# Optimization experiments

Hardware: AMD Instinct MI355X
Metric: run time of the kernel (lower is better)

## Reference

```python
import jax, jax.numpy as jnp
import numpy as np

MUL_S, MUL_V = 256, 128              # 256x0e + 128x1o hidden irreps
DIM_H = MUL_S + 3 * MUL_V            # 640
N_NODES = 100000
INV_SQRT3 = 3.0 ** -0.5
# e3nn 'element' path normalization: sqrt(ir_out.dim / sum_paths(mul1*mul2));
# for the 1o output the extra sqrt(3) cancels the 1/sqrt(3) of the wigner-3j,
# so every path ends up with the same constant.
C0 = (1.0 / (MUL_S + MUL_V)) ** 0.5


def _unif(key, shape, fan):
    # matches linear_layer_init: uniform(-a, a), a = sqrt(6/(mul1*mul2 + mul_out)), mul2 = 1
    a = (6.0 / fan) ** 0.5
    return jax.random.uniform(key, shape, minval=-a, maxval=a, dtype=jnp.float32)


def setup_inputs() -> dict:
    key = jax.random.key(0)
    ks = jax.random.split(key, 8)
    data_in = jax.random.normal(ks[0], (N_NODES, DIM_H + 4), dtype=jnp.float32)
    return {
        "data_in": data_in,
        "W_ss": _unif(ks[1], (MUL_S, MUL_S), MUL_S + MUL_S),      # 0e x 0e -> 0e (scalars)
        "W_vv": _unif(ks[2], (MUL_V, MUL_S), MUL_V + MUL_S),      # 1o x 1o -> 0e (scalars)
        "W_ss_g": _unif(ks[3], (MUL_S, MUL_V), MUL_S + MUL_V),    # 0e x 0e -> 0e (gates)
        "W_vv_g": _unif(ks[4], (MUL_V, MUL_V), MUL_V + MUL_V),    # 1o x 1o -> 0e (gates)
        "W_sv": _unif(ks[5], (MUL_S, MUL_V), MUL_S + MUL_V),      # 0e x 1o -> 1o
        "W_vs": _unif(ks[6], (MUL_V, MUL_V), MUL_V + MUL_V),      # 1o x 0e -> 1o
        "b": jnp.zeros((MUL_S,), dtype=jnp.float32),
    }


def reference(data_in, W_ss, W_vv, W_ss_g, W_vv_g, W_sv, W_vs, b):
    # split hidden / pos parts (forward does data_in[:, :-irreps_pos.dim] etc.)
    xs = data_in[:, :MUL_S]                           # [N, 256] 0e
    xv = data_in[:, MUL_S:DIM_H].reshape(-1, MUL_V, 3)  # [N, 128, 3] 1o
    ps = data_in[:, DIM_H:DIM_H + 1]                  # [N, 1] pos scalar
    pv = data_in[:, DIM_H + 1:]                       # [N, 3] pos vector

    # CG invariants feeding the 0e outputs
    s0 = xs * ps                                       # 0e x 0e path
    dot = jnp.einsum('nuk,nk->nu', xv, pv) * INV_SQRT3  # 1o x 1o -> 0e path, [N, 128]

    scal = C0 * (s0 @ W_ss + dot @ W_vv) + b           # [N, 256] scalars (+bias on N_trivial)
    gate = C0 * (s0 @ W_ss_g + dot @ W_vv_g)           # [N, 128] gates

    # 1o outputs: 0e x 1o and 1o x 0e paths
    v1 = (xs @ W_sv)[:, :, None] * pv[:, None, :]            # [N, 128, 3]
    v2 = jnp.einsum('nuk,uw->nwk', xv, W_vs) * ps[:, :, None]  # [N, 128, 3]
    vec = C0 * (v1 + v2)

    # Gate: Swish(beta=1) on scalars, sigmoid(gates) multiplying gated 1o irreps
    scal_out = scal * jax.nn.sigmoid(scal)
    vec_out = vec * jax.nn.sigmoid(gate)[:, :, None]
    return jnp.concatenate([scal_out, vec_out.reshape(-1, 3 * MUL_V)], axis=1)  # [N, 640]
```

## Files before the change

kernel.cpp:

```cpp
#include <hip/hip_runtime.h>
#include <hip/hip_bf16.h>

#define MUL_Sc 256
#define DIM_Hc 640
#define IN_COLS 644
#define KF 768
#define NT 32

#define C0F 0.05103103630798287f
#define INV_SQRT3F 0.57735026918962576f

typedef __attribute__((ext_vector_type(8))) short short8;
typedef __attribute__((ext_vector_type(4))) float f32x4;

#define MFMA(a, b, c) __builtin_amdgcn_mfma_f32_16x16x32_bf16((a), (b), (c), 0, 0, 0)

__device__ __forceinline__ unsigned short f2bf(float x) {
    union { float f; unsigned u; } v; v.f = x;
    unsigned r = v.u + 0x7fffu + ((v.u >> 16) & 1u);
    return (unsigned short)(r >> 16);
}

__device__ __forceinline__ void gload_lds16(const unsigned short* g, unsigned short* l) {
    __builtin_amdgcn_global_load_lds((const __attribute__((address_space(1))) void*)g,
                                     (__attribute__((address_space(3))) void*)l, 16, 0, 0);
}

__global__ void prep_weights(const float* __restrict__ Wss, const float* __restrict__ Wvv,
                             const float* __restrict__ Wssg, const float* __restrict__ Wvvg,
                             const float* __restrict__ Wsv, const float* __restrict__ Wvs,
                             unsigned short* __restrict__ wt) {
    int i = blockIdx.x * 256 + threadIdx.x;
    const int N_SG = 384 * 384;
    const int N_SV = 128 * 256;
    const int N_VS = 128 * 128;
    if (i < N_SG) {
        int col = i / 384, k = i % 384;
        float v;
        if (col < 256) v = (k < 256) ? Wss[k * 256 + col] : Wvv[(k - 256) * 256 + col];
        else { int c = col - 256; v = (k < 256) ? Wssg[k * 128 + c] : Wvvg[(k - 256) * 128 + c]; }
        wt[i] = f2bf(v);
    } else if (i < N_SG + N_SV) {
        int j = i - N_SG; int col = j >> 8, k = j & 255;
        wt[i] = f2bf(Wsv[k * 128 + col]);
    } else if (i < N_SG + N_SV + N_VS) {
        int j = i - N_SG - N_SV; int col = j >> 7, k = j & 127;
        wt[i] = f2bf(Wvs[k * 128 + col]);
    }
}

__global__ __launch_bounds__(512, 2)
void fused_main(const float* __restrict__ din, const unsigned short* __restrict__ wt,
                const float* __restrict__ bias, float* __restrict__ out, int N) {
    __shared__ unsigned short feat[NT * KF];
    __shared__ unsigned short ldsB[2][384 * 64];
    __shared__ float psv[NT * 4];

    const int tid  = threadIdx.x;
    const int wave = tid >> 6;
    const int lane = tid & 63;
    const int n0   = blockIdx.x * NT;

    const unsigned short* WTsg = wt;
    const unsigned short* WTsv = wt + 384 * 384;
    const unsigned short* WTvs = wt + 384 * 384 + 128 * 256;

    auto stage = [&](int buf, const unsigned short* W, int rs, int nr, int step) {
        unsigned short* lb = &ldsB[buf][0] + wave * 512;
        #pragma unroll
        for (int m = 0; m < nr; ++m) {
            int slot = m * 512 + tid;
            int col  = slot >> 3;
            int k8   = (slot & 7) ^ (col & 7);
            gload_lds16(W + col * rs + step * 64 + k8 * 8, lb + m * 4096);
        }
    };

    stage(0, WTsg, 384, 6, 0);

    {
        const int g = tid >> 4;
        const int j = tid & 15;
        int n = n0 + g; if (n >= N) n = N - 1;
        const float* row = din + (size_t)n * IN_COLS;
        float ps  = row[DIM_Hc];
        float pv0 = row[DIM_Hc + 1], pv1 = row[DIM_Hc + 2], pv2 = row[DIM_Hc + 3];
        if (j == 0) { psv[g*4+0] = ps; psv[g*4+1] = pv0; psv[g*4+2] = pv1; psv[g*4+3] = pv2; }
        char* fb = (char*)feat;
        const int swz  = (g & 7) << 4;
        const int rowb = g * (KF * 2);

        {
            int c = 16 * j;
            float4 x0 = *(const float4*)(row + c);
            float4 x1 = *(const float4*)(row + c + 4);
            float4 x2 = *(const float4*)(row + c + 8);
            float4 x3 = *(const float4*)(row + c + 12);
            short8 p0, p1;
            p0[0]=(short)f2bf(x0.x); p0[1]=(short)f2bf(x0.y); p0[2]=(short)f2bf(x0.z); p0[3]=(short)f2bf(x0.w);
            p0[4]=(short)f2bf(x1.x); p0[5]=(short)f2bf(x1.y); p0[6]=(short)f2bf(x1.z); p0[7]=(short)f2bf(x1.w);
            p1[0]=(short)f2bf(x2.x); p1[1]=(short)f2bf(x2.y); p1[2]=(short)f2bf(x2.z); p1[3]=(short)f2bf(x2.w);
            p1[4]=(short)f2bf(x3.x); p1[5]=(short)f2bf(x3.y); p1[6]=(short)f2bf(x3.z); p1[7]=(short)f2bf(x3.w);
            *(short8*)(fb + ((rowb + c * 2) ^ swz))       = p0;
            *(short8*)(fb + ((rowb + (c + 8) * 2) ^ swz)) = p1;
        }
        {
            int u0 = 8 * j;
            const float* p = row + MUL_Sc + 3 * u0;
            float e[24];
            #pragma unroll
            for (int q = 0; q < 6; ++q) {
                float4 v = *(const float4*)(p + 4 * q);
                e[4*q+0] = v.x; e[4*q+1] = v.y; e[4*q+2] = v.z; e[4*q+3] = v.w;
            }
            short8 dp, k0, k1, k2;
            #pragma unroll
            for (int m = 0; m < 8; ++m) {
                float a = e[3*m], b = e[3*m+1], c = e[3*m+2];
                dp[m] = (short)f2bf((a * pv0 + b * pv1 + c * pv2) * INV_SQRT3F);
                k0[m] = (short)f2bf(a);
                k1[m] = (short)f2bf(b);
                k2[m] = (short)f2bf(c);
            }
            *(short8*)(fb + ((rowb + (256 + u0) * 2) ^ swz)) = dp;
            *(short8*)(fb + ((rowb + (384 + u0) * 2) ^ swz)) = k0;
            *(short8*)(fb + ((rowb + (512 + u0) * 2) ^ swz)) = k1;
            *(short8*)(fb + ((rowb + (640 + u0) * 2) ^ swz)) = k2;
        }
    }
    __syncthreads();

    const int l15   = lane & 15;
    const int lkb   = (lane >> 4) << 3;
    const int chnk  = lane >> 4;
    const int rbase = (lane >> 4) << 2;
    const char* fbr = (const char*)feat;
    const int swzr  = (l15 & 7) << 4;

    float pss[2][4];
    #pragma unroll
    for (int s = 0; s < 2; ++s)
    #pragma unroll
    for (int i = 0; i < 4; ++i) pss[s][i] = psv[(s * 16 + rbase + i) * 4];

    f32x4 accS[3][2];
    #pragma unroll
    for (int t = 0; t < 3; ++t) { accS[t][0] = (f32x4){0,0,0,0}; accS[t][1] = (f32x4){0,0,0,0}; }
    f32x4 accA[2];
    accA[0] = (f32x4){0,0,0,0}; accA[1] = (f32x4){0,0,0,0};
    f32x4 accV[3][2];
    #pragma unroll
    for (int k = 0; k < 3; ++k) { accV[k][0] = (f32x4){0,0,0,0}; accV[k][1] = (f32x4){0,0,0,0}; }

    auto sgstep = [&](int buf, int step) {
        const char* B = (const char*)&ldsB[buf][0];
        #pragma unroll
        for (int ks = 0; ks < 2; ++ks) {
            int kf = step * 64 + ks * 32 + lkb;
            short8 a0 = *(const short8*)(fbr + ((l15 * 1536 + kf * 2) ^ swzr));
            short8 a1 = *(const short8*)(fbr + (((16 + l15) * 1536 + kf * 2) ^ swzr));
            int ch = ks * 4 + chnk;
            #pragma unroll
            for (int t = 0; t < 3; ++t) {
                int col = (wave + t * 8) * 16 + l15;
                short8 b = *(const short8*)(B + col * 128 + ((ch ^ (col & 7)) << 4));
                accS[t][0] = MFMA(a0, b, accS[t][0]);
                accS[t][1] = MFMA(a1, b, accS[t][1]);
            }
        }
    };
    auto svstep = [&](int buf, int step) {
        const char* B = (const char*)&ldsB[buf][0];
        #pragma unroll
        for (int ks = 0; ks < 2; ++ks) {
            int kf = step * 64 + ks * 32 + lkb;
            short8 a0 = *(const short8*)(fbr + ((l15 * 1536 + kf * 2) ^ swzr));
            short8 a1 = *(const short8*)(fbr + (((16 + l15) * 1536 + kf * 2) ^ swzr));
            int ch = ks * 4 + chnk;
            int col = wave * 16 + l15;
            short8 b = *(const short8*)(B + col * 128 + ((ch ^ (col & 7)) << 4));
            accA[0] = MFMA(a0, b, accA[0]);
            accA[1] = MFMA(a1, b, accA[1]);
        }
    };
    auto vsstep = [&](int buf, int step) {
        const char* B = (const char*)&ldsB[buf][0];
        #pragma unroll
        for (int ks = 0; ks < 2; ++ks) {
            int ch = ks * 4 + chnk;
            int col = wave * 16 + l15;
            short8 b = *(const short8*)(B + col * 128 + ((ch ^ (col & 7)) << 4));
            #pragma unroll
            for (int p = 0; p < 3; ++p) {
                int kf = 384 + p * 128 + step * 64 + ks * 32 + lkb;
                short8 a0 = *(const short8*)(fbr + ((l15 * 1536 + kf * 2) ^ swzr));
                short8 a1 = *(const short8*)(fbr + (((16 + l15) * 1536 + kf * 2) ^ swzr));
                accV[p][0] = MFMA(a0, b, accV[p][0]);
                accV[p][1] = MFMA(a1, b, accV[p][1]);
            }
        }
    };

    stage(1, WTsg, 384, 6, 1);  sgstep(0, 0);  __syncthreads();
    stage(0, WTsg, 384, 6, 2);  sgstep(1, 1);  __syncthreads();
    stage(1, WTsg, 384, 6, 3);  sgstep(0, 2);  __syncthreads();
    stage(0, WTsg, 384, 6, 4);  sgstep(1, 3);
    #pragma unroll
    for (int t = 0; t < 3; ++t)
    #pragma unroll
    for (int s = 0; s < 2; ++s)
    #pragma unroll
    for (int i = 0; i < 4; ++i) accS[t][s][i] *= pss[s][i];
    __syncthreads();
    stage(1, WTsg, 384, 6, 5);  sgstep(0, 4);  __syncthreads();
    stage(0, WTsv, 256, 2, 0);  sgstep(1, 5);

    #pragma unroll
    for (int t = 0; t < 2; ++t) {
        int col = (wave + t * 8) * 16 + l15;
        float bc = bias[col];
        #pragma unroll
        for (int s = 0; s < 2; ++s)
        #pragma unroll
        for (int i = 0; i < 4; ++i) {
            int n = n0 + s * 16 + rbase + i;
            if (n < N) {
                float sc = C0F * accS[t][s][i] + bc;
                out[(size_t)n * DIM_Hc + col] = sc / (1.f + __expf(-sc));
            }
        }
    }
    float sgr[2][4];
    #pragma unroll
    for (int s = 0; s < 2; ++s)
    #pragma unroll
    for (int i = 0; i < 4; ++i) sgr[s][i] = 1.f / (1.f + __expf(-C0F * accS[2][s][i]));
    __syncthreads();

    stage(1, WTsv, 256, 2, 1);  svstep(0, 0);  __syncthreads();
    stage(0, WTsv, 256, 2, 2);  svstep(1, 1);  __syncthreads();
    stage(1, WTsv, 256, 2, 3);  svstep(0, 2);  __syncthreads();
    stage(0, WTvs, 128, 2, 0);  svstep(1, 3);  __syncthreads();
    stage(1, WTvs, 128, 2, 1);  vsstep(0, 0);  __syncthreads();
                                vsstep(1, 1);

    {
        int u = wave * 16 + l15;
        #pragma unroll
        for (int s = 0; s < 2; ++s)
        #pragma unroll
        for (int i = 0; i < 4; ++i) {
            int nl = s * 16 + rbase + i;
            int n = n0 + nl;
            if (n >= N) continue;
            float sg  = sgr[s][i];
            float ps  = pss[s][i];
            float pv0 = psv[nl * 4 + 1], pv1 = psv[nl * 4 + 2], pv2 = psv[nl * 4 + 3];
            float av = accA[s][i];
            size_t ob = (size_t)n * DIM_Hc + MUL_Sc + 3 * u;
            out[ob + 0] = C0F * (av * pv0 + accV[0][s][i] * ps) * sg;
            out[ob + 1] = C0F * (av * pv1 + accV[1][s][i] * ps) * sg;
            out[ob + 2] = C0F * (av * pv2 + accV[2][s][i] * ps) * sg;
        }
    }
}

extern "C" void kernel_launch(void* const* d_in, const int* in_sizes, int n_in,
                              void* d_out, int out_size, void* d_ws, size_t ws_size,
                              hipStream_t stream) {
    const float* din  = (const float*)d_in[0];
    const float* Wss  = (const float*)d_in[1];
    const float* Wvv  = (const float*)d_in[2];
    const float* Wssg = (const float*)d_in[3];
    const float* Wvvg = (const float*)d_in[4];
    const float* Wsv  = (const float*)d_in[5];
    const float* Wvs  = (const float*)d_in[6];
    const float* bias = (const float*)d_in[7];
    float* out = (float*)d_out;
    unsigned short* wt = (unsigned short*)d_ws;

    const size_t WT_BYTES = (size_t)(384 * 384 + 128 * 256 + 128 * 128) * 2;
    if (ws_size < WT_BYTES) return;

    int N = in_sizes[0] / IN_COLS;

    int prep_total = 384 * 384 + 128 * 256 + 128 * 128;
    prep_weights<<<(prep_total + 255) / 256, 256, 0, stream>>>(Wss, Wvv, Wssg, Wvvg, Wsv, Wvs, wt);

    int nblocks = (N + NT - 1) / NT;
    fused_main<<<nblocks, 512, 0, stream>>>(din, wt, bias, out, N);
}
```

Before: 269.3 us.

## Use persistent producer/consumer blocks with double-buffered feature tiles and direct global weight reads

Launches a fixed grid of 256 persistent blocks that loop over 32-node tiles. Half the threads act as producers, converting and staging the next tile's features into a second LDS buffer, while the other four waves run the MFMA work on the current tile. Weights are no longer staged through LDS; consumers read B fragments straight from global memory (L2/L1 cached), and each consumer wave now handles twice the columns. This aims to overlap input loading with compute and remove the per-step weight-staging barriers. In exchange, only half the threads issue MFMAs, and there is more global-load latency on the weight operand.

After: 333.8 us. +24.0%, slower.

```diff
diff --git a/kernel.cpp b/kernel.cpp
--- a/kernel.cpp
+++ b/kernel.cpp
@@ -6,6 +6,7 @@
 #define IN_COLS 644
 #define KF 768
 #define NT 32
+#define GRIDB 256
 
 #define C0F 0.05103103630798287f
 #define INV_SQRT3F 0.57735026918962576f
@@ -19,11 +20,6 @@
     union { float f; unsigned u; } v; v.f = x;
     unsigned r = v.u + 0x7fffu + ((v.u >> 16) & 1u);
     return (unsigned short)(r >> 16);
-}
-
-__device__ __forceinline__ void gload_lds16(const unsigned short* g, unsigned short* l) {
-    __builtin_amdgcn_global_load_lds((const __attribute__((address_space(1))) void*)g,
-                                     (__attribute__((address_space(3))) void*)l, 16, 0, 0);
 }
 
 __global__ void prep_weights(const float* __restrict__ Wss, const float* __restrict__ Wvv,
@@ -51,217 +47,229 @@
 
 __global__ __launch_bounds__(512, 2)
 void fused_main(const float* __restrict__ din, const unsigned short* __restrict__ wt,
-                const float* __restrict__ bias, float* __restrict__ out, int N) {
-    __shared__ unsigned short feat[NT * KF];
-    __shared__ unsigned short ldsB[2][384 * 64];
-    __shared__ float psv[NT * 4];
+                const float* __restrict__ bias, float* __restrict__ out,
+                int N, int ntiles) {
+    __shared__ unsigned short feat[2][NT * KF];
+    __shared__ float psv[2][NT * 4];
 
     const int tid  = threadIdx.x;
-    const int wave = tid >> 6;
-    const int lane = tid & 63;
-    const int n0   = blockIdx.x * NT;
+    const bool prod = tid >= 256;
+    const int ptid = tid & 255;
 
     const unsigned short* WTsg = wt;
     const unsigned short* WTsv = wt + 384 * 384;
     const unsigned short* WTvs = wt + 384 * 384 + 128 * 256;
 
-    auto stage = [&](int buf, const unsigned short* W, int rs, int nr, int step) {
-        unsigned short* lb = &ldsB[buf][0] + wave * 512;
+    const int cw    = tid >> 6;
+    const int lane  = tid & 63;
+    const int l15   = lane & 15;
+    const int lkb   = (lane >> 4) << 3;
+    const int rbase = (lane >> 4) << 2;
+    const int swzr  = (l15 & 7) << 4;
+
+    float bcs[4];
+    if (!prod) {
         #pragma unroll
-        for (int m = 0; m < nr; ++m) {
-            int slot = m * 512 + tid;
-            int col  = slot >> 3;
-            int k8   = (slot & 7) ^ (col & 7);
-            gload_lds16(W + col * rs + step * 64 + k8 * 8, lb + m * 4096);
+        for (int t = 0; t < 4; ++t) bcs[t] = bias[(t * 4 + cw) * 16 + l15];
+    }
+
+    auto stage_tile = [&](int tile, int wb) {
+        char* fb = (char*)&feat[wb][0];
+        #pragma unroll
+        for (int h = 0; h < 2; ++h) {
+            const int g = h * 16 + (ptid >> 4);
+            const int j = ptid & 15;
+            int n = tile * NT + g; if (n >= N) n = N - 1;
+            const float* row = din + (size_t)n * IN_COLS;
+            float ps  = row[DIM_Hc];
+            float pv0 = row[DIM_Hc + 1], pv1 = row[DIM_Hc + 2], pv2 = row[DIM_Hc + 3];
+            if (j == 0) {
+                psv[wb][g*4+0] = ps; psv[wb][g*4+1] = pv0;
+                psv[wb][g*4+2] = pv1; psv[wb][g*4+3] = pv2;
+            }
+            const int swz  = (g & 7) << 4;
+            const int rowb = g * (KF * 2);
+
+            {
+                int c = 16 * j;
+                float4 x0 = *(const float4*)(row + c);
+                float4 x1 = *(const float4*)(row + c + 4);
+                float4 x2 = *(const float4*)(row + c + 8);
+                float4 x3 = *(const float4*)(row + c + 12);
+                short8 p0, p1;
+                p0[0]=(short)f2bf(x0.x); p0[1]=(short)f2bf(x0.y); p0[2]=(short)f2bf(x0.z); p0[3]=(short)f2bf(x0.w);
+                p0[4]=(short)f2bf(x1.x); p0[5]=(short)f2bf(x1.y); p0[6]=(short)f2bf(x1.z); p0[7]=(short)f2bf(x1.w);
+                p1[0]=(short)f2bf(x2.x); p1[1]=(short)f2bf(x2.y); p1[2]=(short)f2bf(x2.z); p1[3]=(short)f2bf(x2.w);
+                p1[4]=(short)f2bf(x3.x); p1[5]=(short)f2bf(x3.y); p1[6]=(short)f2bf(x3.z); p1[7]=(short)f2bf(x3.w);
+                *(short8*)(fb + ((rowb + c * 2) ^ swz))       = p0;
+                *(short8*)(fb + ((rowb + (c + 8) * 2) ^ swz)) = p1;
+            }
+            {
+                int u0 = 8 * j;
+                const float* p = row + MUL_Sc + 3 * u0;
+                float e[24];
+                #pragma unroll
+                for (int q = 0; q < 6; ++q) {
+                    float4 v = *(const float4*)(p + 4 * q);
+                    e[4*q+0] = v.x; e[4*q+1] = v.y; e[4*q+2] = v.z; e[4*q+3] = v.w;
+                }
+                short8 dp, k0, k1, k2;
+                #pragma unroll
+                for (int m = 0; m < 8; ++m) {
+                    float a = e[3*m], b = e[3*m+1], c = e[3*m+2];
+                    dp[m] = (short)f2bf((a * pv0 + b * pv1 + c * pv2) * INV_SQRT3F);
+                    k0[m] = (short)f2bf(a);
+                    k1[m] = (short)f2bf(b);
+                    k2[m] = (short)f2bf(c);
+                }
+                *(short8*)(fb + ((rowb + (256 + u0) * 2) ^ swz)) = dp;
+                *(short8*)(fb + ((rowb + (384 + u0) * 2) ^ swz)) = k0;
+                *(short8*)(fb + ((rowb + (512 + u0) * 2) ^ swz)) = k1;
+                *(short8*)(fb + ((rowb + (640 + u0) * 2) ^ swz)) = k2;
+            }
         }
     };
 
-    stage(0, WTsg, 384, 6, 0);
-
-    {
-        const int g = tid >> 4;
-        const int j = tid & 15;
-        int n = n0 + g; if (n >= N) n = N - 1;
-        const float* row = din + (size_t)n * IN_COLS;
-        float ps  = row[DIM_Hc];
-        float pv0 = row[DIM_Hc + 1], pv1 = row[DIM_Hc + 2], pv2 = row[DIM_Hc + 3];
-        if (j == 0) { psv[g*4+0] = ps; psv[g*4+1] = pv0; psv[g*4+2] = pv1; psv[g*4+3] = pv2; }
-        char* fb = (char*)feat;
-        const int swz  = (g & 7) << 4;
-        const int rowb = g * (KF * 2);
-
-        {
-            int c = 16 * j;
-            float4 x0 = *(const float4*)(row + c);
-            float4 x1 = *(const float4*)(row + c + 4);
-            float4 x2 = *(const float4*)(row + c + 8);
-            float4 x3 = *(const float4*)(row + c + 12);
-            short8 p0, p1;
-            p0[0]=(short)f2bf(x0.x); p0[1]=(short)f2bf(x0.y); p0[2]=(short)f2bf(x0.z); p0[3]=(short)f2bf(x0.w);
-            p0[4]=(short)f2bf(x1.x); p0[5]=(short)f2bf(x1.y); p0[6]=(short)f2bf(x1.z); p0[7]=(short)f2bf(x1.w);
-            p1[0]=(short)f2bf(x2.x); p1[1]=(short)f2bf(x2.y); p1[2]=(short)f2bf(x2.z); p1[3]=(short)f2bf(x2.w);
-            p1[4]=(short)f2bf(x3.x); p1[5]=(short)f2bf(x3.y); p1[6]=(short)f2bf(x3.z); p1[7]=(short)f2bf(x3.w);
-            *(short8*)(fb + ((rowb + c * 2) ^ swz))       = p0;
-            *(short8*)(fb + ((rowb + (c + 8) * 2) ^ swz)) = p1;
-        }
-        {
-            int u0 = 8 * j;
-            const float* p = row + MUL_Sc + 3 * u0;
-            float e[24];
-            #pragma unroll
-            for (int q = 0; q < 6; ++q) {
-                float4 v = *(const float4*)(p + 4 * q);
-                e[4*q+0] = v.x; e[4*q+1] = v.y; e[4*q+2] = v.z; e[4*q+3] = v.w;
-            }
-            short8 dp, k0, k1, k2;
-            #pragma unroll
-            for (int m = 0; m < 8; ++m) {
-                float a = e[3*m], b = e[3*m+1], c = e[3*m+2];
-                dp[m] = (short)f2bf((a * pv0 + b * pv1 + c * pv2) * INV_SQRT3F);
-                k0[m] = (short)f2bf(a);
-                k1[m] = (short)f2bf(b);
-                k2[m] = (short)f2bf(c);
-            }
-            *(short8*)(fb + ((rowb + (256 + u0) * 2) ^ swz)) = dp;
-            *(short8*)(fb + ((rowb + (384 + u0) * 2) ^ swz)) = k0;
-            *(short8*)(fb + ((rowb + (512 + u0) * 2) ^ swz)) = k1;
-            *(short8*)(fb + ((rowb + (640 + u0) * 2) ^ swz)) = k2;
-        }
-    }
+    if (prod) stage_tile(blockIdx.x, 0);
     __syncthreads();
 
-    const int l15   = lane & 15;
-    const int lkb   = (lane >> 4) << 3;
-    const int chnk  = lane >> 4;
-    const int rbase = (lane >> 4) << 2;
-    const char* fbr = (const char*)feat;
-    const int swzr  = (l15 & 7) << 4;
-
-    float pss[2][4];
-    #pragma unroll
-    for (int s = 0; s < 2; ++s)
-    #pragma unroll
-    for (int i = 0; i < 4; ++i) pss[s][i] = psv[(s * 16 + rbase + i) * 4];
-
-    f32x4 accS[3][2];
-    #pragma unroll
-    for (int t = 0; t < 3; ++t) { accS[t][0] = (f32x4){0,0,0,0}; accS[t][1] = (f32x4){0,0,0,0}; }
-    f32x4 accA[2];
-    accA[0] = (f32x4){0,0,0,0}; accA[1] = (f32x4){0,0,0,0};
-    f32x4 accV[3][2];
-    #pragma unroll
-    for (int k = 0; k < 3; ++k) { accV[k][0] = (f32x4){0,0,0,0}; accV[k][1] = (f32x4){0,0,0,0}; }
-
-    auto sgstep = [&](int buf, int step) {
-        const char* B = (const char*)&ldsB[buf][0];
-        #pragma unroll
-        for (int ks = 0; ks < 2; ++ks) {
-            int kf = step * 64 + ks * 32 + lkb;
-            short8 a0 = *(const short8*)(fbr + ((l15 * 1536 + kf * 2) ^ swzr));
-            short8 a1 = *(const short8*)(fbr + (((16 + l15) * 1536 + kf * 2) ^ swzr));
-            int ch = ks * 4 + chnk;
-            #pragma unroll
-            for (int t = 0; t < 3; ++t) {
-                int col = (wave + t * 8) * 16 + l15;
-                short8 b = *(const short8*)(B + col * 128 + ((ch ^ (col & 7)) << 4));
-                accS[t][0] = MFMA(a0, b, accS[t][0]);
-                accS[t][1] = MFMA(a1, b, accS[t][1]);
-            }
-        }
-    };
-    auto svstep = [&](int buf, int step) {
-        const char* B = (const char*)&ldsB[buf][0];
-        #pragma unroll
-        for (int ks = 0; ks < 2; ++ks) {
-            int kf = step * 64 + ks * 32 + lkb;
-            short8 a0 = *(const short8*)(fbr + ((l15 * 1536 + kf * 2) ^ swzr));
-            short8 a1 = *(const short8*)(fbr + (((16 + l15) * 1536 + kf * 2) ^ swzr));
-            int ch = ks * 4 + chnk;
-            int col = wave * 16 + l15;
-            short8 b = *(const short8*)(B + col * 128 + ((ch ^ (col & 7)) << 4));
-            accA[0] = MFMA(a0, b, accA[0]);
-            accA[1] = MFMA(a1, b, accA[1]);
-        }
-    };
-    auto vsstep = [&](int buf, int step) {
-        const char* B = (const char*)&ldsB[buf][0];
-        #pragma unroll
-        for (int ks = 0; ks < 2; ++ks) {
-            int ch = ks * 4 + chnk;
-            int col = wave * 16 + l15;
-            short8 b = *(const short8*)(B + col * 128 + ((ch ^ (col & 7)) << 4));
-            #pragma unroll
-            for (int p = 0; p < 3; ++p) {
-                int kf = 384 + p * 128 + step * 64 + ks * 32 + lkb;
+    int wbuf = 0;
+    for (int tile = blockIdx.x; tile < ntiles; tile += GRIDB) {
+        if (prod) {
+            int nx = tile + GRIDB;
+            if (nx < ntiles) stage_tile(nx, wbuf ^ 1);
+        } else {
+            const char* fbr = (const char*)&feat[wbuf][0];
+            const float* pvv = &psv[wbuf][0];
+            const int n0 = tile * NT;
+
+            float pss[2][4];
+            #pragma unroll
+            for (int m = 0; m < 2; ++m)
+            #pragma unroll
+            for (int i = 0; i < 4; ++i) pss[m][i] = pvv[(m * 16 + rbase + i) * 4];
+
+            f32x4 accS[6][2];
+            #pragma unroll
+            for (int t = 0; t < 6; ++t) { accS[t][0] = (f32x4){0,0,0,0}; accS[t][1] = (f32x4){0,0,0,0}; }
+
+            #pragma unroll
+            for (int ks = 0; ks < 8; ++ks) {
+                int kf = ks * 32 + lkb;
                 short8 a0 = *(const short8*)(fbr + ((l15 * 1536 + kf * 2) ^ swzr));
                 short8 a1 = *(const short8*)(fbr + (((16 + l15) * 1536 + kf * 2) ^ swzr));
-                accV[p][0] = MFMA(a0, b, accV[p][0]);
-                accV[p][1] = MFMA(a1, b, accV[p][1]);
+                #pragma unroll
+                for (int t = 0; t < 6; ++t) {
+                    int col = (t * 4 + cw) * 16 + l15;
+                    short8 b = *(const short8*)(WTsg + col * 384 + ks * 32 + lkb);
+                    accS[t][0] = MFMA(a0, b, accS[t][0]);
+                    accS[t][1] = MFMA(a1, b, accS[t][1]);
+                }
+            }
+            #pragma unroll
+            for (int t = 0; t < 6; ++t)
+            #pragma unroll
+            for (int m = 0; m < 2; ++m)
+            #pragma unroll
+            for (int i = 0; i < 4; ++i) accS[t][m][i] *= pss[m][i];
+            #pragma unroll
+            for (int ks = 0; ks < 4; ++ks) {
+                int kf = 256 + ks * 32 + lkb;
+                short8 a0 = *(const short8*)(fbr + ((l15 * 1536 + kf * 2) ^ swzr));
+                short8 a1 = *(const short8*)(fbr + (((16 + l15) * 1536 + kf * 2) ^ swzr));
+                #pragma unroll
+                for (int t = 0; t < 6; ++t) {
+                    int col = (t * 4 + cw) * 16 + l15;
+                    short8 b = *(const short8*)(WTsg + col * 384 + 256 + ks * 32 + lkb);
+                    accS[t][0] = MFMA(a0, b, accS[t][0]);
+                    accS[t][1] = MFMA(a1, b, accS[t][1]);
+                }
+            }
+
+            #pragma unroll
+            for (int t = 0; t < 4; ++t) {
+                int col = (t * 4 + cw) * 16 + l15;
+                #pragma unroll
+                for (int m = 0; m < 2; ++m)
+                #pragma unroll
+                for (int i = 0; i < 4; ++i) {
+                    int n = n0 + m * 16 + rbase + i;
+                    if (n < N) {
+                        float sc = C0F * accS[t][m][i] + bcs[t];
+                        out[(size_t)n * DIM_Hc + col] = sc / (1.f + __expf(-sc));
+                    }
+                }
+            }
+            float sgr[2][2][4];
+            #pragma unroll
+            for (int s = 0; s < 2; ++s)
+            #pragma unroll
+            for (int m = 0; m < 2; ++m)
+            #pragma unroll
+            for (int i = 0; i < 4; ++i) sgr[s][m][i] = 1.f / (1.f + __expf(-C0F * accS[4 + s][m][i]));
+
+            f32x4 accA[2][2], accV[3][2][2];
+            #pragma unroll
+            for (int s = 0; s < 2; ++s) {
+                accA[s][0] = (f32x4){0,0,0,0}; accA[s][1] = (f32x4){0,0,0,0};
+                #pragma unroll
+                for (int k = 0; k < 3; ++k) { accV[k][s][0] = (f32x4){0,0,0,0}; accV[k][s][1] = (f32x4){0,0,0,0}; }
+            }
+            #pragma unroll
+            for (int ks = 0; ks < 8; ++ks) {
+                int kf = ks * 32 + lkb;
+                short8 a0 = *(const short8*)(fbr + ((l15 * 1536 + kf * 2) ^ swzr));
+                short8 a1 = *(const short8*)(fbr + (((16 + l15) * 1536 + kf * 2) ^ swzr));
+                #pragma unroll
+                for (int s = 0; s < 2; ++s) {
+                    int ucol = (s * 4 + cw) * 16 + l15;
+                    short8 b = *(const short8*)(WTsv + ucol * 256 + ks * 32 + lkb);
+                    accA[s][0] = MFMA(a0, b, accA[s][0]);
+                    accA[s][1] = MFMA(a1, b, accA[s][1]);
+                }
+            }
+            #pragma unroll
+            for (int ks = 0; ks < 4; ++ks) {
+                short8 bv[2];
+                #pragma unroll
+                for (int s = 0; s < 2; ++s)
+                    bv[s] = *(const short8*)(WTvs + ((s * 4 + cw) * 16 + l15) * 128 + ks * 32 + lkb);
+                #pragma unroll
+                for (int p = 0; p < 3; ++p) {
+                    int kf = 384 + 128 * p + ks * 32 + lkb;
+                    short8 a0 = *(const short8*)(fbr + ((l15 * 1536 + kf * 2) ^ swzr));
+                    short8 a1 = *(const short8*)(fbr + (((16 + l15) * 1536 + kf * 2) ^ swzr));
+                    #pragma unroll
+                    for (int s = 0; s < 2; ++s) {
+                        accV[p][s][0] = MFMA(a0, bv[s], accV[p][s][0]);
+                        accV[p][s][1] = MFMA(a1, bv[s], accV[p][s][1]);
+                    }
+                }
+            }
+
+            #pragma unroll
+            for (int s = 0; s < 2; ++s) {
+                int u = (s * 4 + cw) * 16 + l15;
+                #pragma unroll
+                for (int m = 0; m < 2; ++m)
+                #pragma unroll
+                for (int i = 0; i < 4; ++i) {
+                    int nl = m * 16 + rbase + i;
+                    int n = n0 + nl;
+                    if (n >= N) continue;
+                    float sg  = sgr[s][m][i];
+                    float ps  = pss[m][i];
+                    float pv0 = pvv[nl * 4 + 1], pv1 = pvv[nl * 4 + 2], pv2 = pvv[nl * 4 + 3];
+                    float av = accA[s][m][i];
+                    size_t ob = (size_t)n * DIM_Hc + MUL_Sc + 3 * u;
+                    out[ob + 0] = C0F * (av * pv0 + accV[0][s][m][i] * ps) * sg;
+                    out[ob + 1] = C0F * (av * pv1 + accV[1][s][m][i] * ps) * sg;
+                    out[ob + 2] = C0F * (av * pv2 + accV[2][s][m][i] * ps) * sg;
+                }
             }
         }
-    };
-
-    stage(1, WTsg, 384, 6, 1);  sgstep(0, 0);  __syncthreads();
-    stage(0, WTsg, 384, 6, 2);  sgstep(1, 1);  __syncthreads();
-    stage(1, WTsg, 384, 6, 3);  sgstep(0, 2);  __syncthreads();
-    stage(0, WTsg, 384, 6, 4);  sgstep(1, 3);
-    #pragma unroll
-    for (int t = 0; t < 3; ++t)
-    #pragma unroll
-    for (int s = 0; s < 2; ++s)
-    #pragma unroll
-    for (int i = 0; i < 4; ++i) accS[t][s][i] *= pss[s][i];
-    __syncthreads();
-    stage(1, WTsg, 384, 6, 5);  sgstep(0, 4);  __syncthreads();
-    stage(0, WTsv, 256, 2, 0);  sgstep(1, 5);
-
-    #pragma unroll
-    for (int t = 0; t < 2; ++t) {
-        int col = (wave + t * 8) * 16 + l15;
-        float bc = bias[col];
-        #pragma unroll
-        for (int s = 0; s < 2; ++s)
-        #pragma unroll
-        for (int i = 0; i < 4; ++i) {
-            int n = n0 + s * 16 + rbase + i;
-            if (n < N) {
-                float sc = C0F * accS[t][s][i] + bc;
-                out[(size_t)n * DIM_Hc + col] = sc / (1.f + __expf(-sc));
-            }
-        }
-    }
-    float sgr[2][4];
-    #pragma unroll
-    for (int s = 0; s < 2; ++s)
-    #pragma unroll
-    for (int i = 0; i < 4; ++i) sgr[s][i] = 1.f / (1.f + __expf(-C0F * accS[2][s][i]));
-    __syncthreads();
-
-    stage(1, WTsv, 256, 2, 1);  svstep(0, 0);  __syncthreads();
-    stage(0, WTsv, 256, 2, 2);  svstep(1, 1);  __syncthreads();
-    stage(1, WTsv, 256, 2, 3);  svstep(0, 2);  __syncthreads();
-    stage(0, WTvs, 128, 2, 0);  svstep(1, 3);  __syncthreads();
-    stage(1, WTvs, 128, 2, 1);  vsstep(0, 0);  __syncthreads();
-                                vsstep(1, 1);
-
-    {
-        int u = wave * 16 + l15;
-        #pragma unroll
-        for (int s = 0; s < 2; ++s)
-        #pragma unroll
-        for (int i = 0; i < 4; ++i) {
-            int nl = s * 16 + rbase + i;
-            int n = n0 + nl;
-            if (n >= N) continue;
-            float sg  = sgr[s][i];
-            float ps  = pss[s][i];
-            float pv0 = psv[nl * 4 + 1], pv1 = psv[nl * 4 + 2], pv2 = psv[nl * 4 + 3];
-            float av = accA[s][i];
-            size_t ob = (size_t)n * DIM_Hc + MUL_Sc + 3 * u;
-            out[ob + 0] = C0F * (av * pv0 + accV[0][s][i] * ps) * sg;
-            out[ob + 1] = C0F * (av * pv1 + accV[1][s][i] * ps) * sg;
-            out[ob + 2] = C0F * (av * pv2 + accV[2][s][i] * ps) * sg;
-        }
+        __syncthreads();
+        wbuf ^= 1;
     }
 }
 
@@ -283,10 +291,10 @@
     if (ws_size < WT_BYTES) return;
 
     int N = in_sizes[0] / IN_COLS;
+    int ntiles = (N + NT - 1) / NT;
 
     int prep_total = 384 * 384 + 128 * 256 + 128 * 128;
     prep_weights<<<(prep_total + 255) / 256, 256, 0, stream>>>(Wss, Wvv, Wssg, Wvvg, Wsv, Wvs, wt);
 
-    int nblocks = (N + NT - 1) / NT;
-    fused_main<<<nblocks, 512, 0, stream>>>(din, wt, bias, out, N);
+    fused_main<<<GRIDB, 512, 0, stream>>>(din, wt, bias, out, N, ntiles);
 }
```
